# Optimization experiments

Measured on AMD Instinct MI355X. Metric: run time of the kernel, lower is better.

The kernel has to match this reference:

```python
import jax, jax.numpy as jnp
import numpy as np

B, L, D, NLAYERS, MAX_NODES, DEG = 32, 512, 768, 3, 128, 8


def _build_graph():
    rng = np.random.default_rng(0)
    per = rng.integers(-32, 33, size=B // 2)
    sizes = np.concatenate([96 + per, 96 - per]).astype(np.int64)  # sum = 96*B = 3072, each in [64,128]
    N = int(sizes.sum())
    offs = np.concatenate([[0], np.cumsum(sizes)])
    batch = np.repeat(np.arange(B), sizes).astype(np.int64)
    pad_idx = np.zeros((B, MAX_NODES), np.int64)
    pad_mask = np.zeros((B, MAX_NODES), bool)
    src, dst = [], []
    for b in range(B):
        n = int(sizes[b])
        pad_idx[b, :n] = np.arange(offs[b], offs[b] + n)
        pad_mask[b, :n] = True
        src.append(rng.integers(offs[b], offs[b] + n, n * DEG))
        dst.append(rng.integers(offs[b], offs[b] + n, n * DEG))
    return N, batch, pad_idx, pad_mask, np.concatenate(src), np.concatenate(dst)


def setup_inputs() -> dict:
    N, batch, pad_idx, pad_mask, esrc, edst = _build_graph()
    key = jax.random.key(0)
    ks = jax.random.split(key, 8)
    s = 1.0 / np.sqrt(D)
    return {
        "x": jax.random.normal(ks[0], (N, D), jnp.float32),
        "text": jax.random.normal(ks[1], (B, L, D), jnp.float32),
        "batch_ent1_d_mask": jnp.ones((B, 1), jnp.float32),
        "batch_ent1_g_mask": jnp.ones((B, 1), jnp.float32),
        "gnn_ws": jax.random.normal(ks[2], (NLAYERS, D, D), jnp.float32) * s,
        "gnn_wn": jax.random.normal(ks[3], (NLAYERS, D, D), jnp.float32) * s,
        "gnn_b": jnp.zeros((NLAYERS, D), jnp.float32),
        "atom_w": jax.random.normal(ks[4], (D, D), jnp.float32) * s,
        "atom_b": jnp.zeros((D,), jnp.float32),
        "rand_emb": jax.random.normal(ks[5], (1, D), jnp.float32),
        "batch": jnp.asarray(batch),
        "pad_idx": jnp.asarray(pad_idx),
        "pad_mask": jnp.asarray(pad_mask),
        "edge_src": jnp.asarray(esrc),
        "edge_dst": jnp.asarray(edst),
    }


def reference(x, text, batch_ent1_d_mask, batch_ent1_g_mask, gnn_ws, gnn_wn, gnn_b,
              atom_w, atom_b, rand_emb, batch, pad_idx, pad_mask, edge_src, edge_dst):
    N = x.shape[0]
    E = edge_src.shape[0]
    maskf = pad_mask.astype(x.dtype)            # [B, M]
    n_per = maskf.sum(axis=1)                   # [B] num real nodes per graph
    # edge-neighbor mean counts (constants w.r.t. x)
    cnt = jax.ops.segment_sum(jnp.ones((E,), x.dtype), edge_dst, num_segments=N)
    inv_cnt = 1.0 / jnp.maximum(cnt, 1.0)
    cms = []
    for i in range(NLAYERS):
        # MoleGraphConv stand-in: mean neighbor aggregation + self transform
        msg = jax.ops.segment_sum(x[edge_src], edge_dst, num_segments=N) * inv_cnt[:, None]
        x = jax.nn.relu(x @ gnn_ws[i] + msg @ gnn_wn[i] + gnn_b[i])
        # ragged gather into padded [B, M, D]
        xp = x[pad_idx] * maskf[..., None]
        # graph -> text cross attention (softmax over text tokens; no mask needed)
        g2t = jax.nn.softmax(jnp.einsum('bmd,bld->bml', xp, text), axis=-1)
        g2t_out = jnp.einsum('bml,bld->bmd', g2t, text)            # [B, M, D]
        # text -> graph cross attention (mask padded nodes)
        t2g_logits = jnp.einsum('bld,bmd->blm', text, xp)
        t2g_logits = jnp.where(pad_mask[:, None, :], t2g_logits, jnp.float32(-1e9))
        t2g = jax.nn.softmax(t2g_logits, axis=-1)
        t2g_out = jnp.einsum('blm,bmd->bld', t2g, xp)              # [B, L, D]
        # mean over concatenated rows [n_i + L] per graph (pool_type=2)
        pooled = ((g2t_out * maskf[..., None]).sum(axis=1) + t2g_out.sum(axis=1)) \
                 / (n_per + jnp.float32(L))[:, None]
        cms.append(pooled)
    out_cms = jnp.mean(jnp.stack(cms, axis=1), axis=1)              # mean over layers
    out_t = text[:, 0, :]
    # scatter-mean of final node features per graph
    gsum = jax.ops.segment_sum(x, batch, num_segments=B)
    gcnt = jax.ops.segment_sum(jnp.ones((N,), x.dtype), batch, num_segments=B)
    xg = gsum / jnp.maximum(gcnt, 1.0)[:, None]
    # dropout is a no-op in eval mode
    out_g = jnp.tanh(xg @ atom_w + atom_b)
    z = rand_emb[0]
    dg = batch_ent1_d_mask * batch_ent1_g_mask
    return jnp.concatenate([
        out_t * batch_ent1_d_mask + (1 - batch_ent1_d_mask) * z,
        out_g * batch_ent1_g_mask + (1 - batch_ent1_g_mask) * z,
        out_cms * dg + (1 - dg) * z,
    ], axis=-1)
```

## Files before the change

kernel.cpp:

```cpp
#include <hip/hip_runtime.h>

#define D 768
#define B 32
#define L 512
#define M 128
#define NNODES 3072
#define NEDGES 24576

using bf16x8 = __attribute__((ext_vector_type(8))) short;
using f32x4  = __attribute__((ext_vector_type(4))) float;

__device__ __forceinline__ float bf2f(unsigned short u) {
  union { unsigned int i; float f; } v; v.i = ((unsigned int)u) << 16; return v.f;
}
__device__ __forceinline__ unsigned short f2bf(float f) {
  union { float f; unsigned int i; } v; v.f = f;
  unsigned int x = v.i;
  return (unsigned short)((x + 0x7FFFu + ((x >> 16) & 1u)) >> 16);
}
__device__ __forceinline__ float ldf(const void* p, size_t i, int f32) {
  return f32 ? ((const float*)p)[i] : bf2f(((const unsigned short*)p)[i]);
}
__device__ __forceinline__ int ldi(const void* p, size_t i, int w64) {
  return w64 ? (int)((const long long*)p)[i] : ((const int*)p)[i];
}
__device__ __forceinline__ f32x4 mfma16(bf16x8 a, bf16x8 b, f32x4 c) {
  return __builtin_amdgcn_mfma_f32_16x16x32_bf16(a, b, c, 0, 0, 0);
}
__device__ __forceinline__ void gl_lds(const unsigned short* gsrc, unsigned short* lbase,
                                       int lane) {
  __builtin_amdgcn_global_load_lds(
      (const __attribute__((address_space(1))) unsigned int*)(gsrc + lane * 8),
      (__attribute__((address_space(3))) unsigned int*)lbase, 16, 0, 0);
}

__device__ __forceinline__ float pk_read(const unsigned short* P, int p, int l, int d) {
  return bf2f(P[(((size_t)(p * 24 + (d >> 5))) << 9) + ((((d & 31) >> 3) << 4) + l) * 8 + (d & 7)]);
}

__device__ __forceinline__ void fma8(float* acc, float w, uint4 v) {
  unsigned xs[4] = {v.x, v.y, v.z, v.w};
#pragma unroll
  for (int j = 0; j < 4; ++j) {
    acc[2 * j]     += w * bf2f((unsigned short)(xs[j] & 0xFFFFu));
    acc[2 * j + 1] += w * bf2f((unsigned short)(xs[j] >> 16));
  }
}


__device__ void d_pack_in(const void* src, unsigned short* rows, unsigned short* dst,
                          int p, int tid, int f) {
  unsigned short* pb = dst + (size_t)p * 12288;
#pragma unroll
  for (int j = 0; j < 6; ++j) {
    int odx = j * 256 + tid;
    int kk = odx >> 6, lanep = odx & 63;
    int q = lanep >> 4, r16 = lanep & 15;
    int row = p * 16 + r16, col0 = kk * 32 + q * 8;
    size_t sbase = (size_t)row * 768 + col0;
    union { unsigned short v[8]; uint4 qv; } u;
    if (f) {
      const float* sp = (const float*)src + sbase;
      float4 v0 = *(const float4*)sp;
      float4 v1 = *(const float4*)(sp + 4);
      u.v[0] = f2bf(v0.x); u.v[1] = f2bf(v0.y); u.v[2] = f2bf(v0.z); u.v[3] = f2bf(v0.w);
      u.v[4] = f2bf(v1.x); u.v[5] = f2bf(v1.y); u.v[6] = f2bf(v1.z); u.v[7] = f2bf(v1.w);
    } else {
      u.qv = *(const uint4*)((const unsigned short*)src + sbase);
    }
    if (rows) *(uint4*)&rows[sbase] = u.qv;
    *(uint4*)&pb[(size_t)odx * 8] = u.qv;
  }
}

__device__ void d_pack(const unsigned short* src, unsigned short* dst,
                       int p, int tid) {
  unsigned short* pb = dst + (size_t)p * 12288;
#pragma unroll
  for (int j = 0; j < 6; ++j) {
    int odx = j * 256 + tid;
    int kk = odx >> 6, lanep = odx & 63;
    int q = lanep >> 4, r16 = lanep & 15;
    size_t sbase = (size_t)(p * 16 + r16) * 768 + kk * 32 + q * 8;
    uint4 qv = *(const uint4*)(src + sbase);
    *(uint4*)&pb[(size_t)odx * 8] = qv;
  }
}

__device__ void d_wpack(const void* Ws, const void* Wn, const void* Aw, int f,
                        unsigned short* WsPk, unsigned short* WnPk, unsigned short* AwPk,
                        int r0, int tid, char* smem) {
  unsigned short* buf = (unsigned short*)smem;
  int z = r0 / 288, rem = r0 % 288;
  int nblk = rem % 12, kk = rem / 12;
  const void* src; unsigned short* dst; size_t zoff;
  if (z < 3)      { src = Ws; zoff = (size_t)z * D * D;       dst = WsPk + zoff; }
  else if (z < 6) { src = Wn; zoff = (size_t)(z - 3) * D * D; dst = WnPk + zoff; }
  else            { src = Aw; zoff = 0;                       dst = AwPk; }
  int n0 = nblk * 64;
  int kl = tid >> 3, c8 = tid & 7;
  size_t sbase = zoff + (size_t)(kk * 32 + kl) * D + n0 + c8 * 8;
  unsigned short v[8];
  if (f) {
    const float* sp = (const float*)src + sbase;
#pragma unroll
    for (int e = 0; e < 8; ++e) v[e] = f2bf(sp[e]);
  } else {
    const unsigned short* sp = (const unsigned short*)src + sbase;
#pragma unroll
    for (int e = 0; e < 8; ++e) v[e] = sp[e];
  }
  int ebit = kl & 7, quad = kl >> 3;
#pragma unroll
  for (int i = 0; i < 8; ++i) {
    int nl = c8 * 8 + i;
    int pl = nl >> 4;
    int lane = quad * 16 + (nl & 15);
    buf[pl * 512 + lane * 8 + ebit] = v[i];
  }
  __syncthreads();
  int pl = tid >> 6, pos = tid & 63;
  int pG = nblk * 4 + pl;
  uint4 q = *(const uint4*)&buf[pl * 512 + pos * 8];
  *(uint4*)&dst[(((size_t)(pG * 24 + kk)) << 9) + pos * 8] = q;
}

__device__ void d_count(const void* edst, const void* batch, int w,
                        int* cnt, int* gcnt, int i) {
  if (i < NEDGES) atomicAdd(&cnt[ldi(edst, i, w)], 1);
  if (i < NNODES) atomicAdd(&gcnt[ldi(batch, i, w)], 1);
}

__device__ void d_msg(const unsigned short* x, const int* cnt, const int* rowstart,
                      const int* csr, unsigned short* Mpk, int p, int tid) {
  int w = tid >> 6, lane = tid & 63;
  unsigned short* pb = Mpk + (size_t)p * 12288;
#pragma unroll
  for (int i = 0; i < 4; ++i) {
    int r = w * 4 + i;
    int n = p * 16 + r;
    int deg = cnt[n], base = rowstart[n];
    float inv = 1.0f / (float)(deg > 1 ? deg : 1);
    float a[12];
#pragma unroll
    for (int j = 0; j < 12; ++j) a[j] = 0.f;
    for (int e = 0; e < deg; ++e) {
      const uint2* xr = (const uint2*)(x + (size_t)csr[base + e] * D);
#pragma unroll
      for (int j = 0; j < 3; ++j) {
        uint2 v = xr[lane + j * 64];
        a[j * 4 + 0] += bf2f((unsigned short)(v.x & 0xFFFFu));
        a[j * 4 + 1] += bf2f((unsigned short)(v.x >> 16));
        a[j * 4 + 2] += bf2f((unsigned short)(v.y & 0xFFFFu));
        a[j * 4 + 3] += bf2f((unsigned short)(v.y >> 16));
      }
    }
#pragma unroll
    for (int j = 0; j < 3; ++j) {
      int d0 = (lane + j * 64) * 4;
      int kk = d0 >> 5, q = (d0 >> 3) & 3, e0 = d0 & 7;
      unsigned int lo = (unsigned int)f2bf(a[j * 4 + 0] * inv)
                      | ((unsigned int)f2bf(a[j * 4 + 1] * inv) << 16);
      unsigned int hi = (unsigned int)f2bf(a[j * 4 + 2] * inv)
                      | ((unsigned int)f2bf(a[j * 4 + 3] * inv) << 16);
      uint2 wv; wv.x = lo; wv.y = hi;
      *(uint2*)&pb[kk * 512 + (q * 16 + r) * 8 + e0] = wv;
    }
  }
}

__device__ void d_gemm(const unsigned short* Xpk, const unsigned short* Mpk,
                       const unsigned short* WsPk, const unsigned short* WnPk,
                       const void* bias, size_t bias_off, int f,
                       unsigned short* Y, int bx, int by, int tid, char* smem) {
  unsigned short* lds = (unsigned short*)smem;
  int wave = tid >> 6, lane = tid & 63;
  int q = lane >> 4, t = lane & 15;
  int wm = wave >> 1, wn = wave & 1;
  int pa = bx * 4, pb = by * 4;
  f32x4 acc[2][2];
#pragma unroll
  for (int mi = 0; mi < 2; ++mi)
#pragma unroll
    for (int ni = 0; ni < 2; ++ni)
      acc[mi][ni] = (f32x4){0.f, 0.f, 0.f, 0.f};
  int c0 = wave * 2;
  int pan0 = (wave < 2) ? (pa + c0) : (pb + c0 - 4);
  auto issue = [&](int r) {
    unsigned short* dbuf = &lds[(r % 3) * 8192 + c0 * 512];
#pragma unroll
    for (int st = 0; st < 2; ++st) {
      int s = r * 2 + st;
      int h = (s >= 24) ? 1 : 0;
      const unsigned short* P = (wave < 2) ? (h ? Mpk : Xpk) : (h ? WnPk : WsPk);
      int kk = s - h * 24;
      gl_lds(P + (((size_t)(pan0 * 24 + kk)) << 9), dbuf + st * 4096, lane);
      gl_lds(P + (((size_t)((pan0 + 1) * 24 + kk)) << 9), dbuf + st * 4096 + 512, lane);
    }
  };
  issue(0);
  issue(1);
  for (int r = 0; r < 24; ++r) {
    if (r < 23) asm volatile("s_waitcnt vmcnt(4)" ::: "memory");
    else        asm volatile("s_waitcnt vmcnt(0)" ::: "memory");
    __builtin_amdgcn_s_barrier();
    asm volatile("" ::: "memory");
    if (r < 22) issue(r + 2);
    const unsigned short* bb = &lds[(r % 3) * 8192];
#pragma unroll
    for (int st = 0; st < 2; ++st) {
      const unsigned short* bs = bb + st * 4096;
      bf16x8 a0 = *(const bf16x8*)&bs[(wm * 2 + 0) * 512 + lane * 8];
      bf16x8 a1 = *(const bf16x8*)&bs[(wm * 2 + 1) * 512 + lane * 8];
      bf16x8 b0 = *(const bf16x8*)&bs[(4 + wn * 2 + 0) * 512 + lane * 8];
      bf16x8 b1 = *(const bf16x8*)&bs[(4 + wn * 2 + 1) * 512 + lane * 8];
      acc[0][0] = mfma16(a0, b0, acc[0][0]);
      acc[0][1] = mfma16(a0, b1, acc[0][1]);
      acc[1][0] = mfma16(a1, b0, acc[1][0]);
      acc[1][1] = mfma16(a1, b1, acc[1][1]);
    }
    asm volatile("" ::: "memory");
  }
#pragma unroll
  for (int ni = 0; ni < 2; ++ni) {
    int col = by * 64 + wn * 32 + ni * 16 + t;
    float bv = ldf(bias, bias_off + col, f);
#pragma unroll
    for (int mi = 0; mi < 2; ++mi) {
#pragma unroll
      for (int r = 0; r < 4; ++r) {
        int row = bx * 64 + wm * 32 + mi * 16 + q * 4 + r;
        float v = acc[mi][ni][r] + bv;
        Y[(size_t)row * D + col] = f2bf(v > 0.f ? v : 0.f);
      }
    }
  }
}

__device__ void d_xp(const unsigned short* Xn, const void* pidx, int w64,
                     const int* gcnt, unsigned short* xp, unsigned short* XpPk,
                     float* xgacc, int p, int tid, char* smem) {
  unsigned short* rows = (unsigned short*)smem;
  int r = tid >> 4, c16 = tid & 15;
  int bm = p * 16 + r;
  int b = bm >> 7, m = bm & 127;
  int nb = gcnt[b];
  uint4* dl = (uint4*)&rows[r * 776];
  if (m < nb) {
    const uint4* srcr = (const uint4*)(Xn + (size_t)ldi(pidx, bm, w64) * D);
#pragma unroll
    for (int j = 0; j < 6; ++j) dl[c16 + j * 16] = srcr[c16 + j * 16];
  } else {
    uint4 z = {0u, 0u, 0u, 0u};
#pragma unroll
    for (int j = 0; j < 6; ++j) dl[c16 + j * 16] = z;
  }
  __syncthreads();
#pragma unroll
  for (int j = 0; j < 6; ++j) {
    int idx = j * 256 + tid;
    int rr = idx / 96, cc = idx % 96;
    uint4 vv = *(const uint4*)&rows[rr * 776 + cc * 8];
    *(uint4*)&xp[(size_t)(p * 16 + rr) * D + cc * 8] = vv;
  }
  unsigned short* pb = XpPk + (size_t)p * 12288;
#pragma unroll
  for (int j = 0; j < 6; ++j) {
    int odx = j * 256 + tid;
    int kk = odx >> 6, lanep = odx & 63;
    int rr = lanep & 15, cg = lanep >> 4;
    int cc = kk * 4 + cg;
    uint4 vv = *(const uint4*)&rows[rr * 776 + cc * 8];
    *(uint4*)&pb[odx * 8] = vv;
  }
  if (xgacc) {
    int bb = p >> 3;
#pragma unroll
    for (int j = 0; j < 3; ++j) {
      int d = j * 256 + tid;
      float s = 0.f;
#pragma unroll
      for (int rr = 0; rr < 16; ++rr) s += bf2f(rows[rr * 776 + d]);
      atomicAdd(&xgacc[(size_t)bb * D + d], s);
    }
  }
}

__device__ void d_scores(const unsigned short* XpPk, const unsigned short* Tpk,
                         float* S, int bx, int by, int bz, int tid, char* smem) {
  unsigned short* lds = (unsigned short*)smem;
  int wave = tid >> 6, lane = tid & 63;
  int q = lane >> 4, t = lane & 15;
  int wm = wave >> 1, wn = wave & 1;
  int pa = bz * 8 + bx * 4;
  int pb = bz * 32 + by * 4;
  f32x4 acc[2][2];
#pragma unroll
  for (int mi = 0; mi < 2; ++mi)
#pragma unroll
    for (int ni = 0; ni < 2; ++ni)
      acc[mi][ni] = (f32x4){0.f, 0.f, 0.f, 0.f};
  int c0 = wave * 2;
  const unsigned short* P = (wave < 2) ? XpPk : Tpk;
  int pan0 = (wave < 2) ? (pa + c0) : (pb + c0 - 4);
  auto issue = [&](int r) {
    unsigned short* dbuf = &lds[(r % 3) * 8192 + c0 * 512];
#pragma unroll
    for (int st = 0; st < 2; ++st) {
      int kk = r * 2 + st;
      gl_lds(P + (((size_t)(pan0 * 24 + kk)) << 9), dbuf + st * 4096, lane);
      gl_lds(P + (((size_t)((pan0 + 1) * 24 + kk)) << 9), dbuf + st * 4096 + 512, lane);
    }
  };
  issue(0);
  issue(1);
  for (int r = 0; r < 12; ++r) {
    if (r < 11) asm volatile("s_waitcnt vmcnt(4)" ::: "memory");
    else        asm volatile("s_waitcnt vmcnt(0)" ::: "memory");
    __builtin_amdgcn_s_barrier();
    asm volatile("" ::: "memory");
    if (r < 10) issue(r + 2);
    const unsigned short* bb = &lds[(r % 3) * 8192];
#pragma unroll
    for (int st = 0; st < 2; ++st) {
      const unsigned short* bs = bb + st * 4096;
      bf16x8 a0 = *(const bf16x8*)&bs[(wm * 2 + 0) * 512 + lane * 8];
      bf16x8 a1 = *(const bf16x8*)&bs[(wm * 2 + 1) * 512 + lane * 8];
      bf16x8 b0 = *(const bf16x8*)&bs[(4 + wn * 2 + 0) * 512 + lane * 8];
      bf16x8 b1 = *(const bf16x8*)&bs[(4 + wn * 2 + 1) * 512 + lane * 8];
      acc[0][0] = mfma16(a0, b0, acc[0][0]);
      acc[0][1] = mfma16(a0, b1, acc[0][1]);
      acc[1][0] = mfma16(a1, b0, acc[1][0]);
      acc[1][1] = mfma16(a1, b1, acc[1][1]);
    }
    asm volatile("" ::: "memory");
  }
  float* Sb = S + (size_t)bz * M * L;
#pragma unroll
  for (int ni = 0; ni < 2; ++ni) {
    int col = by * 64 + wn * 32 + ni * 16 + t;
#pragma unroll
    for (int mi = 0; mi < 2; ++mi) {
#pragma unroll
      for (int r = 0; r < 4; ++r) {
        int row = bx * 64 + wm * 32 + mi * 16 + q * 4 + r;
        Sb[(size_t)row * L + col] = acc[mi][ni][r];
      }
    }
  }
}

__device__ void d_stats(const float* S, const int* gcnt, float* rmax, float* rsum,
                        float* cmaxv, float* csumv, int bid, int tid, char* smem) {
  if (bid < B * M) {
    float* red = (float*)smem;
    int lane = tid & 63, wv = tid >> 6;
    const float* r = S + (size_t)bid * L;
    float s0 = r[tid], s1 = r[tid + 256];
    float m = fmaxf(s0, s1);
#pragma unroll
    for (int o = 32; o > 0; o >>= 1) m = fmaxf(m, __shfl_down(m, o));
    if (lane == 0) red[wv] = m;
    __syncthreads();
    float bm = fmaxf(fmaxf(red[0], red[1]), fmaxf(red[2], red[3]));
    __syncthreads();
    float e = __expf(s0 - bm) + __expf(s1 - bm);
#pragma unroll
    for (int o = 32; o > 0; o >>= 1) e += __shfl_down(e, o);
    if (lane == 0) red[wv] = e;
    __syncthreads();
    if (tid == 0) { rmax[bid] = bm; rsum[bid] = red[0] + red[1] + red[2] + red[3]; }
  } else {
    float (*pm)[64] = (float(*)[64])smem;
    float (*ps)[64] = (float(*)[64])(smem + 1024);
    int cid = bid - B * M;
    int b = cid >> 3, ly = cid & 7;
    int w = tid >> 6, lane = tid & 63;
    int l = ly * 64 + lane;
    int nb = gcnt[b];
    const float* Sb = S + (size_t)b * M * L;
    int m0 = w * 32, m1 = min(m0 + 32, nb);
    float cm = -1e30f, cs = 0.f;
    for (int m = m0; m < m1; ++m) {
      float s = Sb[(size_t)m * L + l];
      if (s > cm) { cs = cs * __expf(cm - s) + 1.f; cm = s; }
      else cs += __expf(s - cm);
    }
    pm[w][lane] = cm; ps[w][lane] = cs;
    __syncthreads();
    if (w == 0) {
      float CM = -1e30f;
#pragma unroll
      for (int j = 0; j < 4; ++j) CM = fmaxf(CM, pm[j][lane]);
      float CS = 0.f;
#pragma unroll
      for (int j = 0; j < 4; ++j) CS += ps[j][lane] * __expf(pm[j][lane] - CM);
      cmaxv[b * L + l] = CM; csumv[b * L + l] = CS;
    }
  }
}

__device__ void d_cross(const float* S, const float* rmax, const float* rsum,
                        const float* cmaxv, const float* csumv, const int* gcnt,
                        float* wv, float* t2gcol, int bid, int tid, char* smem) {
  if (bid < 256) {
    float* rm = (float*)smem;
    float* ri = (float*)(smem + 512);
    float (*pw)[64] = (float(*)[64])(smem + 1024);
    int b = bid >> 3, ly = bid & 7;
    int w = tid >> 6, lane = tid & 63;
    if (tid < M) { rm[tid] = rmax[b * M + tid]; ri[tid] = 1.f / rsum[b * M + tid]; }
    __syncthreads();
    int l = ly * 64 + lane;
    int nb = gcnt[b];
    const float* Sb = S + (size_t)b * M * L;
    int m0 = w * 32, m1 = min(m0 + 32, nb);
    float wp = 0.f;
    for (int m = m0; m < m1; ++m)
      wp += __expf(Sb[(size_t)m * L + l] - rm[m]) * ri[m];
    pw[w][lane] = wp;
    __syncthreads();
    if (w == 0)
      wv[b * L + l] = pw[0][lane] + pw[1][lane] + pw[2][lane] + pw[3][lane];
  } else {
    float* red = (float*)smem;
    int bm = bid - 256;
    int b = bm >> 7, m = bm & 127;
    int lane = tid & 63, w = tid >> 6;
    int nb = gcnt[b];
    float acc = 0.f;
    if (m < nb) {
      const float* r = S + (size_t)bm * L;
      const float* cm = cmaxv + b * L;
      const float* cs = csumv + b * L;
      acc = __expf(r[tid] - cm[tid]) / cs[tid]
          + __expf(r[tid + 256] - cm[tid + 256]) / cs[tid + 256];
    }
#pragma unroll
    for (int o = 32; o > 0; o >>= 1) acc += __shfl_down(acc, o);
    if (lane == 0) red[w] = acc;
    __syncthreads();
    if (tid == 0) t2gcol[bm] = red[0] + red[1] + red[2] + red[3];
  }
}

__device__ void d_pooled(const float* wv, const float* t2gcol, const unsigned short* Tpk,
                         const unsigned short* xp, const int* gcnt, float* pooled,
                         int bid, int tid, char* smem) {
  float* lred = (float*)smem;
  float* wbuf = (float*)(smem + 3072);
  int b = bid / 10, seg = bid - b * 10;
  int chunk = tid % 96, half = tid / 96;
  int d = chunk * 8;
  float acc[8];
#pragma unroll
  for (int j = 0; j < 8; ++j) acc[j] = 0.f;
  if (tid < 64) {
    wbuf[tid] = (seg < 8) ? wv[b * L + seg * 64 + tid]
                          : t2gcol[b * M + (seg - 8) * 64 + tid];
  }
  __syncthreads();
  if (half < 2) {
    if (seg < 8) {
      int pbase = b * 32 + seg * 4;
      size_t cbase = ((size_t)(d >> 5)) << 9;
      int coff = ((d & 31) >> 3) << 4;
      for (int i = 0; i < 32; ++i) {
        int l = half * 32 + i;
        const unsigned short* src =
            Tpk + (((size_t)((pbase + (l >> 4)) * 24)) << 9) + cbase +
            (size_t)(coff + (l & 15)) * 8;
        fma8(acc, wbuf[l], *(const uint4*)src);
      }
    } else {
      const unsigned short* Xb = xp + (size_t)b * M * D + d;
      int m0 = (seg - 8) * 64;
      for (int i = 0; i < 32; ++i) {
        int mm = half * 32 + i;
        fma8(acc, wbuf[mm], *(const uint4*)&Xb[(size_t)(m0 + mm) * D]);
      }
    }
  }
  if (half == 1) {
#pragma unroll
    for (int j = 0; j < 8; ++j) lred[chunk * 8 + j] = acc[j];
  }
  __syncthreads();
  if (half == 0) {
    float inv = 1.f / ((float)gcnt[b] + 512.f);
#pragma unroll
    for (int j = 0; j < 8; ++j)
      atomicAdd(&pooled[(size_t)b * D + d + j], (acc[j] + lred[chunk * 8 + j]) * inv);
  }
}

__device__ void d_atom(const float* xgacc, const int* gcnt, const unsigned short* AwPk,
                       float* gpre, int bid, int tid) {
  int w = tid >> 6, lane = tid & 63;
  int q = lane >> 4, t = lane & 15;
  int nbase = bid * 64 + w * 16;
  int pb = nbase >> 4;
  int n0 = gcnt[t], n1 = gcnt[16 + t];
  float inv0 = 1.f / (float)(n0 > 1 ? n0 : 1);
  float inv1 = 1.f / (float)(n1 > 1 ? n1 : 1);
  f32x4 acc[2];
  acc[0] = (f32x4){0.f, 0.f, 0.f, 0.f};
  acc[1] = (f32x4){0.f, 0.f, 0.f, 0.f};
  for (int kk = 0; kk < 24; ++kk) {
    const float* s0 = xgacc + (size_t)t * D + kk * 32 + q * 8;
    const float* s1 = xgacc + (size_t)(16 + t) * D + kk * 32 + q * 8;
    union { unsigned short v[8]; bf16x8 f; } a0, a1;
#pragma unroll
    for (int j = 0; j < 8; ++j) { a0.v[j] = f2bf(s0[j] * inv0); a1.v[j] = f2bf(s1[j] * inv1); }
    bf16x8 bv = *(const bf16x8*)(AwPk + (((size_t)(pb * 24 + kk)) << 9) + (lane << 3));
    acc[0] = mfma16(a0.f, bv, acc[0]);
    acc[1] = mfma16(a1.f, bv, acc[1]);
  }
#pragma unroll
  for (int mi = 0; mi < 2; ++mi)
#pragma unroll
    for (int r = 0; r < 4; ++r) {
      int row = mi * 16 + q * 4 + r;
      gpre[(size_t)row * D + nbase + t] = acc[mi][r];
    }
}


__global__ void k_init(int* cnt, int* cursor, int* gcnt, float* pooled, float* xgacc,
                       const unsigned short* __restrict__ t,
                       const unsigned int* __restrict__ e, int* __restrict__ flags) {
  int i = blockIdx.x * 256 + threadIdx.x;
  if (i < NNODES) { cnt[i] = 0; cursor[i] = 0; }
  if (i < B) gcnt[i] = 0;
  if (i < B * D) { pooled[i] = 0.f; xgacc[i] = 0.f; }
  if (blockIdx.x == 0) {
    __shared__ int r0[256];
    __shared__ unsigned r1[256];
    int tid = threadIdx.x;
    int bad = 0;
    for (int j = tid; j < 8192; j += 256) {
      unsigned short u = t[2 * j];
      unsigned ex = (u >> 7) & 0xFF;
      if (ex >= 0xC0) bad = 1;
    }
    unsigned o = 0;
    for (int j = tid; j < NEDGES / 2; j += 256) o |= e[2 * j + 1];
    r0[tid] = bad; r1[tid] = o;
    __syncthreads();
    for (int s = 128; s > 0; s >>= 1) {
      if (tid < s) { r0[tid] |= r0[tid + s]; r1[tid] |= r1[tid + s]; }
      __syncthreads();
    }
    if (tid == 0) { flags[0] = r0[0]; flags[1] = (r1[0] == 0) ? 1 : 0; }
  }
}

__global__ __launch_bounds__(256) void k_setup2(
    const void* x_in, unsigned short* x0, unsigned short* PkA,
    const void* text, unsigned short* Tpk,
    const void* Ws, const void* Wn, const void* Aw,
    unsigned short* WsPk, unsigned short* WnPk, unsigned short* AwPk,
    const void* edst, const void* batch, int* cnt, int* gcnt,
    const int* __restrict__ flags) {
  extern __shared__ char smem[];
  int bid = blockIdx.x, tid = threadIdx.x;
  if (bid < 1216) {
    int f = flags[0];
    if (bid < NNODES / 16) d_pack_in(x_in, x0, PkA, bid, tid, f);
    else d_pack_in(text, nullptr, Tpk, bid - NNODES / 16, tid, f);
  } else if (bid < 3232) {
    d_wpack(Ws, Wn, Aw, flags[0], WsPk, WnPk, AwPk, bid - 1216, tid, smem);
  } else {
    d_count(edst, batch, flags[1], cnt, gcnt, (bid - 3232) * 256 + tid);
  }
}

__global__ void k_scan(const int* __restrict__ cnt, int* __restrict__ rowstart) {
  __shared__ int a[NNODES], b[NNODES];
  int tid = threadIdx.x;
  for (int i = tid; i < NNODES; i += 1024) a[i] = cnt[i];
  __syncthreads();
  int* s = a; int* d = b;
  for (int off = 1; off < NNODES; off <<= 1) {
    for (int i = tid; i < NNODES; i += 1024)
      d[i] = s[i] + (i >= off ? s[i - off] : 0);
    __syncthreads();
    int* t = s; s = d; d = t;
  }
  for (int i = tid; i < NNODES; i += 1024) rowstart[i + 1] = s[i];
  if (tid == 0) rowstart[0] = 0;
}

__global__ void k_scatter(const void* __restrict__ esrc, const void* __restrict__ edst,
                          const int* __restrict__ flags, const int* __restrict__ rowstart,
                          int* __restrict__ cursor, int* __restrict__ csr) {
  int w = flags[1];
  int i = blockIdx.x * 256 + threadIdx.x;
  if (i < NEDGES) {
    int dd = ldi(edst, i, w);
    int pos = atomicAdd(&cursor[dd], 1);
    csr[rowstart[dd] + pos] = ldi(esrc, i, w);
  }
}

__global__ __launch_bounds__(256) void k_msgp(
    const unsigned short* x, const int* cnt, const int* rowstart, const int* csr,
    unsigned short* Mpk) {
  d_msg(x, cnt, rowstart, csr, Mpk, blockIdx.x, threadIdx.x);
}

__device__ __forceinline__ void gemm_map(int g, int& bx, int& by) {
  int gs = (g % 8) * 72 + g / 8;
  bx = gs / 12; by = gs % 12;
}
__device__ __forceinline__ void sc_map(int g, int& bx, int& by, int& bz) {
  int gs = (g % 8) * 64 + g / 8;
  bx = gs & 1; by = (gs >> 1) & 7; bz = gs >> 4;
}

__global__ __launch_bounds__(256) void k_gemm(
    const unsigned short* Apk, const unsigned short* Mpk,
    const unsigned short* WsPk, const unsigned short* WnPk,
    const void* bias, unsigned long bias_off, const int* flags, unsigned short* Y) {
  extern __shared__ char smem[];
  int bx, by; gemm_map(blockIdx.x, bx, by);
  d_gemm(Apk, Mpk, WsPk, WnPk, bias, bias_off, flags[0], Y, bx, by,
         threadIdx.x, smem);
}

__global__ __launch_bounds__(256) void k_postg(
    const unsigned short* Y, unsigned short* Npk, int packN,
    const void* pidx, const int* flags, const int* gcnt,
    unsigned short* xp, unsigned short* XpPk, float* xgacc) {
  extern __shared__ char smem[];
  int bid = blockIdx.x, tid = threadIdx.x;
  if (bid < packN) d_pack(Y, Npk, bid, tid);
  else d_xp(Y, pidx, flags[1], gcnt, xp, XpPk, xgacc, bid - packN, tid, smem);
}

__global__ __launch_bounds__(256) void k_scmsg(
    const unsigned short* XpPk, const unsigned short* Tpk, float* S,
    int msgN, const unsigned short* x, const int* cnt, const int* rowstart,
    const int* csr, unsigned short* Mpk) {
  extern __shared__ char smem[];
  int bid = blockIdx.x, tid = threadIdx.x;
  if (bid < 512) {
    int bx, by, bz; sc_map(bid, bx, by, bz);
    d_scores(XpPk, Tpk, S, bx, by, bz, tid, smem);
  } else d_msg(x, cnt, rowstart, csr, Mpk, bid - 512, tid);
}

__global__ __launch_bounds__(256) void k_stgemm(
    const float* S, const int* gcnt, float* rmax, float* rsum, float* cmaxv, float* csumv,
    int gemmN, const unsigned short* Apk, const unsigned short* Mpk,
    const unsigned short* WsPk, const unsigned short* WnPk,
    const void* bias, unsigned long bias_off, const int* flags, unsigned short* Y) {
  extern __shared__ char smem[];
  int bid = blockIdx.x, tid = threadIdx.x;
  if (bid < 4352) d_stats(S, gcnt, rmax, rsum, cmaxv, csumv, bid, tid, smem);
  else {
    int bx, by; gemm_map(bid - 4352, bx, by);
    d_gemm(Apk, Mpk, WsPk, WnPk, bias, bias_off, flags[0], Y, bx, by, tid, smem);
  }
}

__global__ __launch_bounds__(256) void k_crpostg(
    const float* S, const float* rmax, const float* rsum, const float* cmaxv,
    const float* csumv, const int* gcnt, float* wv, float* t2gcol,
    int packN, int xpN, const unsigned short* Y, unsigned short* Npk,
    const void* pidx, const int* flags, unsigned short* xp, unsigned short* XpPk,
    float* xgacc) {
  extern __shared__ char smem[];
  int bid = blockIdx.x, tid = threadIdx.x;
  if (bid < 4352) d_cross(S, rmax, rsum, cmaxv, csumv, gcnt, wv, t2gcol, bid, tid, smem);
  else {
    int r = bid - 4352;
    if (r < packN) d_pack(Y, Npk, r, tid);
    else d_xp(Y, pidx, flags[1], gcnt, xp, XpPk, xgacc, r - packN, tid, smem);
  }
}

__global__ __launch_bounds__(256) void k_plscmsg(
    const float* wv, const float* t2gcol, const unsigned short* Tpk,
    const unsigned short* xpL, const int* gcnt, float* pooled,
    int scN, const unsigned short* XpPk, float* S,
    int msgN, const unsigned short* x, const int* cnt, const int* rowstart,
    const int* csr, unsigned short* Mpk,
    int atomN, const float* xgacc, const unsigned short* AwPk, float* gpre) {
  extern __shared__ char smem[];
  int bid = blockIdx.x, tid = threadIdx.x;
  if (bid < 320) { d_pooled(wv, t2gcol, Tpk, xpL, gcnt, pooled, bid, tid, smem); return; }
  int r = bid - 320;
  if (r < scN) {
    int bx, by, bz; sc_map(r, bx, by, bz);
    d_scores(XpPk, Tpk, S, bx, by, bz, tid, smem); return;
  }
  r -= scN;
  if (r < msgN) { d_msg(x, cnt, rowstart, csr, Mpk, r, tid); return; }
  d_atom(xgacc, gcnt, AwPk, gpre, r - msgN, tid);
}

__global__ __launch_bounds__(256) void k_final(
    const unsigned short* __restrict__ Tpk, const float* __restrict__ gpre,
    const float* __restrict__ pooled, const void* __restrict__ ab,
    const void* __restrict__ dmask, const void* __restrict__ gmask,
    const void* __restrict__ remb, const int* __restrict__ flags,
    void* __restrict__ out) {
  int f = flags[0];
  int b = blockIdx.x, tid = threadIdx.x;
  float dm = ldf(dmask, b, f);
  float gm = ldf(gmask, b, f);
  float dg = dm * gm;
  size_t base = (size_t)b * 2304;
#pragma unroll
  for (int j = 0; j < 3; ++j) {
    int d = tid + j * 256;
    float z = ldf(remb, d, f);
    float tv = pk_read(Tpk, b * 32, 0, d);
    float o0 = tv * dm + (1.f - dm) * z;
    float gv = tanhf(gpre[(size_t)b * D + d] + ldf(ab, d, f));
    float o1 = gv * gm + (1.f - gm) * z;
    float p = pooled[(size_t)b * D + d] * (1.f / 3.f);
    float o2 = p * dg + (1.f - dg) * z;
    if (f) {
      float* of = (float*)out;
      of[base + d] = o0; of[base + 768 + d] = o1; of[base + 1536 + d] = o2;
    } else {
      unsigned short* ob = (unsigned short*)out;
      ob[base + d] = f2bf(o0); ob[base + 768 + d] = f2bf(o1); ob[base + 1536 + d] = f2bf(o2);
    }
  }
}

extern "C" void kernel_launch(void* const* d_in, const int* in_sizes, int n_in,
                              void* d_out, int out_size, void* d_ws, size_t ws_size,
                              hipStream_t stream) {
  const void* x_in  = d_in[0];
  const void* text  = d_in[1];
  const void* dmask = d_in[2];
  const void* gmask = d_in[3];
  const void* gws   = d_in[4];
  const void* gwn   = d_in[5];
  const void* gb    = d_in[6];
  const void* aw    = d_in[7];
  const void* ab    = d_in[8];
  const void* remb  = d_in[9];
  const void* batch = d_in[10];
  const void* pidx  = d_in[11];
  const void* esrc  = d_in[13];
  const void* edst  = d_in[14];

  char* wsp = (char*)d_ws;
  size_t off = 0;
  auto carve = [&](size_t bytes) -> void* {
    void* p = wsp + off;
    off += (bytes + 255) & ~(size_t)255;
    return p;
  };
  int* flags = (int*)carve(2 * 4);
  unsigned short* x0    = (unsigned short*)carve((size_t)NNODES * D * 2);
  unsigned short* xA    = (unsigned short*)carve((size_t)NNODES * D * 2);
  unsigned short* xB    = (unsigned short*)carve((size_t)NNODES * D * 2);
  unsigned short* PkA   = (unsigned short*)carve((size_t)NNODES * D * 2);
  unsigned short* PkB   = (unsigned short*)carve((size_t)NNODES * D * 2);
  unsigned short* Mpk   = (unsigned short*)carve((size_t)NNODES * D * 2);
  unsigned short* Tpk   = (unsigned short*)carve((size_t)B * L * D * 2);
  unsigned short* WsPk  = (unsigned short*)carve((size_t)3 * D * D * 2);
  unsigned short* WnPk  = (unsigned short*)carve((size_t)3 * D * D * 2);
  unsigned short* AwPk  = (unsigned short*)carve((size_t)D * D * 2);
  unsigned short* xpA   = (unsigned short*)carve((size_t)B * M * D * 2);
  unsigned short* xpB   = (unsigned short*)carve((size_t)B * M * D * 2);
  unsigned short* XpPkA = (unsigned short*)carve((size_t)B * M * D * 2);
  unsigned short* XpPkB = (unsigned short*)carve((size_t)B * M * D * 2);
  float* xgacc   = (float*)carve((size_t)B * D * 4);
  float* gpre    = (float*)carve((size_t)B * D * 4);
  float* S       = (float*)carve((size_t)B * M * L * 4);
  float* rmax    = (float*)carve((size_t)B * M * 4);
  float* rsum    = (float*)carve((size_t)B * M * 4);
  float* wv      = (float*)carve((size_t)B * L * 4);
  float* cmaxv   = (float*)carve((size_t)B * L * 4);
  float* csumv   = (float*)carve((size_t)B * L * 4);
  float* t2gcol  = (float*)carve((size_t)B * M * 4);
  float* pooled  = (float*)carve((size_t)B * D * 4);
  int* cnt      = (int*)carve((size_t)NNODES * 4);
  int* rowstart = (int*)carve((size_t)(NNODES + 1) * 4);
  int* cursor   = (int*)carve((size_t)NNODES * 4);
  int* gcnt     = (int*)carve((size_t)B * 4);
  int* csr      = (int*)carve((size_t)NEDGES * 4);

  const size_t DD = (size_t)D * D;

  k_init<<<96, 256, 0, stream>>>(cnt, cursor, gcnt, pooled, xgacc,
                                 (const unsigned short*)text, (const unsigned int*)edst, flags);
  k_setup2<<<3328, 256, 4096, stream>>>(x_in, x0, PkA, text, Tpk, gws, gwn, aw,
                                        WsPk, WnPk, AwPk, edst, batch, cnt, gcnt, flags);
  k_scan<<<1, 1024, 0, stream>>>(cnt, rowstart);
  k_scatter<<<96, 256, 0, stream>>>(esrc, edst, flags, rowstart, cursor, csr);

  k_msgp<<<192, 256, 0, stream>>>(x0, cnt, rowstart, csr, Mpk);
  k_gemm<<<576, 256, 49152, stream>>>(PkA, Mpk, WsPk, WnPk, gb, 0, flags, xA);
  k_postg<<<448, 256, 24832, stream>>>(xA, PkB, 192, pidx, flags, gcnt, xpA, XpPkA, nullptr);
  k_scmsg<<<704, 256, 49152, stream>>>(XpPkA, Tpk, S, 192, xA, cnt, rowstart, csr, Mpk);
  k_stgemm<<<4928, 256, 49152, stream>>>(S, gcnt, rmax, rsum, cmaxv, csumv,
                                         576, PkB, Mpk, WsPk + DD, WnPk + DD, gb, D, flags, xB);
  k_crpostg<<<4800, 256, 24832, stream>>>(S, rmax, rsum, cmaxv, csumv, gcnt, wv, t2gcol,
                                          192, 256, xB, PkA, pidx, flags, xpB, XpPkB, nullptr);
  k_plscmsg<<<1024, 256, 49152, stream>>>(wv, t2gcol, Tpk, xpA, gcnt, pooled,
                                          512, XpPkB, S, 192, xB, cnt, rowstart, csr, Mpk,
                                          0, nullptr, nullptr, nullptr);
  k_stgemm<<<4928, 256, 49152, stream>>>(S, gcnt, rmax, rsum, cmaxv, csumv,
                                         576, PkA, Mpk, WsPk + 2 * DD, WnPk + 2 * DD,
                                         gb, 2 * D, flags, xA);
  k_crpostg<<<4608, 256, 24832, stream>>>(S, rmax, rsum, cmaxv, csumv, gcnt, wv, t2gcol,
                                          0, 256, xA, nullptr, pidx, flags, xpA, XpPkA, xgacc);
  k_plscmsg<<<832, 256, 49152, stream>>>(wv, t2gcol, Tpk, xpB, gcnt, pooled,
                                         512, XpPkA, S, 0, nullptr, nullptr, nullptr,
                                         nullptr, nullptr, 0, nullptr, nullptr, nullptr);
  k_stgemm<<<4352, 256, 2048, stream>>>(S, gcnt, rmax, rsum, cmaxv, csumv,
                                        0, nullptr, nullptr, nullptr, nullptr,
                                        nullptr, 0, flags, nullptr);
  k_crpostg<<<4352, 256, 2048, stream>>>(S, rmax, rsum, cmaxv, csumv, gcnt, wv, t2gcol,
                                         0, 0, nullptr, nullptr, pidx, flags,
                                         nullptr, nullptr, nullptr);
  k_plscmsg<<<332, 256, 4096, stream>>>(wv, t2gcol, Tpk, xpA, gcnt, pooled,
                                        0, nullptr, nullptr, 0, nullptr, nullptr, nullptr,
                                        nullptr, nullptr, 12, xgacc, AwPk, gpre);
  k_final<<<32, 256, 0, stream>>>(Tpk, gpre, pooled, ab, dmask, gmask, remb, flags, d_out);
}
```

Baseline: 422.5 us.

## Batch loads for memory parallelism, drop LDS in weight pack, reorder fused block roles

Pack routines now issue all global loads into registers before converting and storing, which raises the number of loads in flight. The weight-pack transpose reads strided columns directly instead of staging through LDS with a barrier, so k_setup2 no longer needs dynamic shared memory. Message aggregation now processes two nodes at once with interleaved neighbor loads. The order of block roles inside the fused kernels changes so that long or latency-bound work (msg, gemm, pack/xp) is scheduled first. In exchange, register pressure rises, and the strided weight reads may coalesce poorly.

After: 434.0 us. 2.7% more time.

```diff
diff --git a/kernel.cpp b/kernel.cpp
--- a/kernel.cpp
+++ b/kernel.cpp
@@ -47,82 +47,99 @@
   }
 }
 
+__device__ __forceinline__ void acc12(float* a, const uint2* u) {
+#pragma unroll
+  for (int j = 0; j < 3; ++j) {
+    a[j * 4 + 0] += bf2f((unsigned short)(u[j].x & 0xFFFFu));
+    a[j * 4 + 1] += bf2f((unsigned short)(u[j].x >> 16));
+    a[j * 4 + 2] += bf2f((unsigned short)(u[j].y & 0xFFFFu));
+    a[j * 4 + 3] += bf2f((unsigned short)(u[j].y >> 16));
+  }
+}
+
 
 __device__ void d_pack_in(const void* src, unsigned short* rows, unsigned short* dst,
                           int p, int tid, int f) {
   unsigned short* pb = dst + (size_t)p * 12288;
+  uint4 qv[6];
+  if (f) {
+    float4 v0[6], v1[6];
+#pragma unroll
+    for (int j = 0; j < 6; ++j) {
+      int odx = j * 256 + tid;
+      int kk = odx >> 6, lanep = odx & 63;
+      size_t sbase = (size_t)(p * 16 + (lanep & 15)) * 768 + kk * 32 + ((lanep >> 4) << 3);
+      const float* sp = (const float*)src + sbase;
+      v0[j] = *(const float4*)sp;
+      v1[j] = *(const float4*)(sp + 4);
+    }
+#pragma unroll
+    for (int j = 0; j < 6; ++j) {
+      union { unsigned short v[8]; uint4 q; } u;
+      u.v[0] = f2bf(v0[j].x); u.v[1] = f2bf(v0[j].y); u.v[2] = f2bf(v0[j].z); u.v[3] = f2bf(v0[j].w);
+      u.v[4] = f2bf(v1[j].x); u.v[5] = f2bf(v1[j].y); u.v[6] = f2bf(v1[j].z); u.v[7] = f2bf(v1[j].w);
+      qv[j] = u.q;
+    }
+  } else {
+#pragma unroll
+    for (int j = 0; j < 6; ++j) {
+      int odx = j * 256 + tid;
+      int kk = odx >> 6, lanep = odx & 63;
+      size_t sbase = (size_t)(p * 16 + (lanep & 15)) * 768 + kk * 32 + ((lanep >> 4) << 3);
+      qv[j] = *(const uint4*)((const unsigned short*)src + sbase);
+    }
+  }
 #pragma unroll
   for (int j = 0; j < 6; ++j) {
     int odx = j * 256 + tid;
     int kk = odx >> 6, lanep = odx & 63;
-    int q = lanep >> 4, r16 = lanep & 15;
-    int row = p * 16 + r16, col0 = kk * 32 + q * 8;
-    size_t sbase = (size_t)row * 768 + col0;
-    union { unsigned short v[8]; uint4 qv; } u;
-    if (f) {
-      const float* sp = (const float*)src + sbase;
-      float4 v0 = *(const float4*)sp;
-      float4 v1 = *(const float4*)(sp + 4);
-      u.v[0] = f2bf(v0.x); u.v[1] = f2bf(v0.y); u.v[2] = f2bf(v0.z); u.v[3] = f2bf(v0.w);
-      u.v[4] = f2bf(v1.x); u.v[5] = f2bf(v1.y); u.v[6] = f2bf(v1.z); u.v[7] = f2bf(v1.w);
-    } else {
-      u.qv = *(const uint4*)((const unsigned short*)src + sbase);
-    }
-    if (rows) *(uint4*)&rows[sbase] = u.qv;
-    *(uint4*)&pb[(size_t)odx * 8] = u.qv;
+    size_t sbase = (size_t)(p * 16 + (lanep & 15)) * 768 + kk * 32 + ((lanep >> 4) << 3);
+    if (rows) *(uint4*)&rows[sbase] = qv[j];
+    *(uint4*)&pb[(size_t)odx * 8] = qv[j];
   }
 }
 
 __device__ void d_pack(const unsigned short* src, unsigned short* dst,
                        int p, int tid) {
   unsigned short* pb = dst + (size_t)p * 12288;
+  uint4 qv[6];
 #pragma unroll
   for (int j = 0; j < 6; ++j) {
     int odx = j * 256 + tid;
     int kk = odx >> 6, lanep = odx & 63;
-    int q = lanep >> 4, r16 = lanep & 15;
-    size_t sbase = (size_t)(p * 16 + r16) * 768 + kk * 32 + q * 8;
-    uint4 qv = *(const uint4*)(src + sbase);
-    *(uint4*)&pb[(size_t)odx * 8] = qv;
+    size_t sbase = (size_t)(p * 16 + (lanep & 15)) * 768 + kk * 32 + ((lanep >> 4) << 3);
+    qv[j] = *(const uint4*)(src + sbase);
+  }
+#pragma unroll
+  for (int j = 0; j < 6; ++j) {
+    *(uint4*)&pb[(size_t)(j * 256 + tid) * 8] = qv[j];
   }
 }
 
 __device__ void d_wpack(const void* Ws, const void* Wn, const void* Aw, int f,
                         unsigned short* WsPk, unsigned short* WnPk, unsigned short* AwPk,
-                        int r0, int tid, char* smem) {
-  unsigned short* buf = (unsigned short*)smem;
+                        int r0, int tid) {
   int z = r0 / 288, rem = r0 % 288;
   int nblk = rem % 12, kk = rem / 12;
   const void* src; unsigned short* dst; size_t zoff;
   if (z < 3)      { src = Ws; zoff = (size_t)z * D * D;       dst = WsPk + zoff; }
   else if (z < 6) { src = Wn; zoff = (size_t)(z - 3) * D * D; dst = WnPk + zoff; }
   else            { src = Aw; zoff = 0;                       dst = AwPk; }
-  int n0 = nblk * 64;
-  int kl = tid >> 3, c8 = tid & 7;
-  size_t sbase = zoff + (size_t)(kk * 32 + kl) * D + n0 + c8 * 8;
-  unsigned short v[8];
+  int pl = tid >> 6, lane = tid & 63;
+  int pG = nblk * 4 + pl;
+  int k0 = kk * 32 + ((lane >> 4) << 3);
+  int n  = nblk * 64 + pl * 16 + (lane & 15);
+  union { unsigned short v[8]; uint4 q; } u;
   if (f) {
-    const float* sp = (const float*)src + sbase;
-#pragma unroll
-    for (int e = 0; e < 8; ++e) v[e] = f2bf(sp[e]);
+    const float* sp = (const float*)src + zoff + (size_t)k0 * D + n;
+#pragma unroll
+    for (int e = 0; e < 8; ++e) u.v[e] = f2bf(sp[(size_t)e * D]);
   } else {
-    const unsigned short* sp = (const unsigned short*)src + sbase;
-#pragma unroll
-    for (int e = 0; e < 8; ++e) v[e] = sp[e];
-  }
-  int ebit = kl & 7, quad = kl >> 3;
-#pragma unroll
-  for (int i = 0; i < 8; ++i) {
-    int nl = c8 * 8 + i;
-    int pl = nl >> 4;
-    int lane = quad * 16 + (nl & 15);
-    buf[pl * 512 + lane * 8 + ebit] = v[i];
-  }
-  __syncthreads();
-  int pl = tid >> 6, pos = tid & 63;
-  int pG = nblk * 4 + pl;
-  uint4 q = *(const uint4*)&buf[pl * 512 + pos * 8];
-  *(uint4*)&dst[(((size_t)(pG * 24 + kk)) << 9) + pos * 8] = q;
+    const unsigned short* sp = (const unsigned short*)src + zoff + (size_t)k0 * D + n;
+#pragma unroll
+    for (int e = 0; e < 8; ++e) u.v[e] = sp[(size_t)e * D];
+  }
+  *(uint4*)&dst[(((size_t)(pG * 24 + kk)) << 9) + lane * 8] = u.q;
 }
 
 __device__ void d_count(const void* edst, const void* batch, int w,
@@ -136,35 +153,45 @@
   int w = tid >> 6, lane = tid & 63;
   unsigned short* pb = Mpk + (size_t)p * 12288;
 #pragma unroll
-  for (int i = 0; i < 4; ++i) {
-    int r = w * 4 + i;
-    int n = p * 16 + r;
-    int deg = cnt[n], base = rowstart[n];
-    float inv = 1.0f / (float)(deg > 1 ? deg : 1);
-    float a[12];
-#pragma unroll
-    for (int j = 0; j < 12; ++j) a[j] = 0.f;
-    for (int e = 0; e < deg; ++e) {
-      const uint2* xr = (const uint2*)(x + (size_t)csr[base + e] * D);
-#pragma unroll
-      for (int j = 0; j < 3; ++j) {
-        uint2 v = xr[lane + j * 64];
-        a[j * 4 + 0] += bf2f((unsigned short)(v.x & 0xFFFFu));
-        a[j * 4 + 1] += bf2f((unsigned short)(v.x >> 16));
-        a[j * 4 + 2] += bf2f((unsigned short)(v.y & 0xFFFFu));
-        a[j * 4 + 3] += bf2f((unsigned short)(v.y >> 16));
+  for (int i = 0; i < 4; i += 2) {
+    int rA = w * 4 + i, rB = rA + 1;
+    int nA = p * 16 + rA, nB = p * 16 + rB;
+    int degA = cnt[nA], baseA = rowstart[nA];
+    int degB = cnt[nB], baseB = rowstart[nB];
+    float aA[12], aB[12];
+#pragma unroll
+    for (int j = 0; j < 12; ++j) { aA[j] = 0.f; aB[j] = 0.f; }
+    int dmax = degA > degB ? degA : degB;
+    for (int e = 0; e < dmax; ++e) {
+      uint2 uA[3], uB[3];
+      if (e < degA) {
+        const uint2* xr = (const uint2*)(x + (size_t)csr[baseA + e] * D);
+        uA[0] = xr[lane]; uA[1] = xr[lane + 64]; uA[2] = xr[lane + 128];
       }
-    }
+      if (e < degB) {
+        const uint2* xr = (const uint2*)(x + (size_t)csr[baseB + e] * D);
+        uB[0] = xr[lane]; uB[1] = xr[lane + 64]; uB[2] = xr[lane + 128];
+      }
+      if (e < degA) acc12(aA, uA);
+      if (e < degB) acc12(aB, uB);
+    }
+    float invA = 1.0f / (float)(degA > 1 ? degA : 1);
+    float invB = 1.0f / (float)(degB > 1 ? degB : 1);
 #pragma unroll
     for (int j = 0; j < 3; ++j) {
       int d0 = (lane + j * 64) * 4;
       int kk = d0 >> 5, q = (d0 >> 3) & 3, e0 = d0 & 7;
-      unsigned int lo = (unsigned int)f2bf(a[j * 4 + 0] * inv)
-                      | ((unsigned int)f2bf(a[j * 4 + 1] * inv) << 16);
-      unsigned int hi = (unsigned int)f2bf(a[j * 4 + 2] * inv)
-                      | ((unsigned int)f2bf(a[j * 4 + 3] * inv) << 16);
-      uint2 wv; wv.x = lo; wv.y = hi;
-      *(uint2*)&pb[kk * 512 + (q * 16 + r) * 8 + e0] = wv;
+      uint2 wA, wB;
+      wA.x = (unsigned int)f2bf(aA[j * 4 + 0] * invA)
+           | ((unsigned int)f2bf(aA[j * 4 + 1] * invA) << 16);
+      wA.y = (unsigned int)f2bf(aA[j * 4 + 2] * invA)
+           | ((unsigned int)f2bf(aA[j * 4 + 3] * invA) << 16);
+      wB.x = (unsigned int)f2bf(aB[j * 4 + 0] * invB)
+           | ((unsigned int)f2bf(aB[j * 4 + 1] * invB) << 16);
+      wB.y = (unsigned int)f2bf(aB[j * 4 + 2] * invB)
+           | ((unsigned int)f2bf(aB[j * 4 + 3] * invB) << 16);
+      *(uint2*)&pb[kk * 512 + (q * 16 + rA) * 8 + e0] = wA;
+      *(uint2*)&pb[kk * 512 + (q * 16 + rB) * 8 + e0] = wB;
     }
   }
 }
@@ -246,15 +273,18 @@
   int b = bm >> 7, m = bm & 127;
   int nb = gcnt[b];
   uint4* dl = (uint4*)&rows[r * 776];
+  uint4 v[6];
   if (m < nb) {
     const uint4* srcr = (const uint4*)(Xn + (size_t)ldi(pidx, bm, w64) * D);
 #pragma unroll
-    for (int j = 0; j < 6; ++j) dl[c16 + j * 16] = srcr[c16 + j * 16];
+    for (int j = 0; j < 6; ++j) v[j] = srcr[c16 + j * 16];
   } else {
     uint4 z = {0u, 0u, 0u, 0u};
 #pragma unroll
-    for (int j = 0; j < 6; ++j) dl[c16 + j * 16] = z;
-  }
+    for (int j = 0; j < 6; ++j) v[j] = z;
+  }
+#pragma unroll
+  for (int j = 0; j < 6; ++j) dl[c16 + j * 16] = v[j];
   __syncthreads();
 #pragma unroll
   for (int j = 0; j < 6; ++j) {
@@ -562,14 +592,13 @@
     unsigned short* WsPk, unsigned short* WnPk, unsigned short* AwPk,
     const void* edst, const void* batch, int* cnt, int* gcnt,
     const int* __restrict__ flags) {
-  extern __shared__ char smem[];
   int bid = blockIdx.x, tid = threadIdx.x;
   if (bid < 1216) {
     int f = flags[0];
     if (bid < NNODES / 16) d_pack_in(x_in, x0, PkA, bid, tid, f);
     else d_pack_in(text, nullptr, Tpk, bid - NNODES / 16, tid, f);
   } else if (bid < 3232) {
-    d_wpack(Ws, Wn, Aw, flags[0], WsPk, WnPk, AwPk, bid - 1216, tid, smem);
+    d_wpack(Ws, Wn, Aw, flags[0], WsPk, WnPk, AwPk, bid - 1216, tid);
   } else {
     d_count(edst, batch, flags[1], cnt, gcnt, (bid - 3232) * 256 + tid);
   }
@@ -634,8 +663,8 @@
     unsigned short* xp, unsigned short* XpPk, float* xgacc) {
   extern __shared__ char smem[];
   int bid = blockIdx.x, tid = threadIdx.x;
-  if (bid < packN) d_pack(Y, Npk, bid, tid);
-  else d_xp(Y, pidx, flags[1], gcnt, xp, XpPk, xgacc, bid - packN, tid, smem);
+  if (bid < 256) d_xp(Y, pidx, flags[1], gcnt, xp, XpPk, xgacc, bid, tid, smem);
+  else d_pack(Y, Npk, bid - 256, tid);
 }
 
 __global__ __launch_bounds__(256) void k_scmsg(
@@ -644,10 +673,11 @@
     const int* csr, unsigned short* Mpk) {
   extern __shared__ char smem[];
   int bid = blockIdx.x, tid = threadIdx.x;
-  if (bid < 512) {
-    int bx, by, bz; sc_map(bid, bx, by, bz);
+  if (bid < msgN) d_msg(x, cnt, rowstart, csr, Mpk, bid, tid);
+  else {
+    int bx, by, bz; sc_map(bid - msgN, bx, by, bz);
     d_scores(XpPk, Tpk, S, bx, by, bz, tid, smem);
-  } else d_msg(x, cnt, rowstart, csr, Mpk, bid - 512, tid);
+  }
 }
 
 __global__ __launch_bounds__(256) void k_stgemm(
@@ -657,11 +687,10 @@
     const void* bias, unsigned long bias_off, const int* flags, unsigned short* Y) {
   extern __shared__ char smem[];
   int bid = blockIdx.x, tid = threadIdx.x;
-  if (bid < 4352) d_stats(S, gcnt, rmax, rsum, cmaxv, csumv, bid, tid, smem);
-  else {
-    int bx, by; gemm_map(bid - 4352, bx, by);
+  if (bid < gemmN) {
+    int bx, by; gemm_map(bid, bx, by);
     d_gemm(Apk, Mpk, WsPk, WnPk, bias, bias_off, flags[0], Y, bx, by, tid, smem);
-  }
+  } else d_stats(S, gcnt, rmax, rsum, cmaxv, csumv, bid - gemmN, tid, smem);
 }
 
 __global__ __launch_bounds__(256) void k_crpostg(
@@ -672,12 +701,10 @@
     float* xgacc) {
   extern __shared__ char smem[];
   int bid = blockIdx.x, tid = threadIdx.x;
-  if (bid < 4352) d_cross(S, rmax, rsum, cmaxv, csumv, gcnt, wv, t2gcol, bid, tid, smem);
-  else {
-    int r = bid - 4352;
-    if (r < packN) d_pack(Y, Npk, r, tid);
-    else d_xp(Y, pidx, flags[1], gcnt, xp, XpPk, xgacc, r - packN, tid, smem);
-  }
+  if (bid < packN) { d_pack(Y, Npk, bid, tid); return; }
+  int r = bid - packN;
+  if (r < xpN) { d_xp(Y, pidx, flags[1], gcnt, xp, XpPk, xgacc, r, tid, smem); return; }
+  d_cross(S, rmax, rsum, cmaxv, csumv, gcnt, wv, t2gcol, r - xpN, tid, smem);
 }
 
 __global__ __launch_bounds__(256) void k_plscmsg(
@@ -689,15 +716,15 @@
     int atomN, const float* xgacc, const unsigned short* AwPk, float* gpre) {
   extern __shared__ char smem[];
   int bid = blockIdx.x, tid = threadIdx.x;
-  if (bid < 320) { d_pooled(wv, t2gcol, Tpk, xpL, gcnt, pooled, bid, tid, smem); return; }
-  int r = bid - 320;
+  if (bid < msgN) { d_msg(x, cnt, rowstart, csr, Mpk, bid, tid); return; }
+  int r = bid - msgN;
   if (r < scN) {
     int bx, by, bz; sc_map(r, bx, by, bz);
     d_scores(XpPk, Tpk, S, bx, by, bz, tid, smem); return;
   }
   r -= scN;
-  if (r < msgN) { d_msg(x, cnt, rowstart, csr, Mpk, r, tid); return; }
-  d_atom(xgacc, gcnt, AwPk, gpre, r - msgN, tid);
+  if (r < 320) { d_pooled(wv, t2gcol, Tpk, xpL, gcnt, pooled, r, tid, smem); return; }
+  d_atom(xgacc, gcnt, AwPk, gpre, r - 320, tid);
 }
 
 __global__ __launch_bounds__(256) void k_final(
@@ -792,8 +819,8 @@
 
   k_init<<<96, 256, 0, stream>>>(cnt, cursor, gcnt, pooled, xgacc,
                                  (const unsigned short*)text, (const unsigned int*)edst, flags);
-  k_setup2<<<3328, 256, 4096, stream>>>(x_in, x0, PkA, text, Tpk, gws, gwn, aw,
-                                        WsPk, WnPk, AwPk, edst, batch, cnt, gcnt, flags);
+  k_setup2<<<3328, 256, 0, stream>>>(x_in, x0, PkA, text, Tpk, gws, gwn, aw,
+                                     WsPk, WnPk, AwPk, edst, batch, cnt, gcnt, flags);
   k_scan<<<1, 1024, 0, stream>>>(cnt, rowstart);
   k_scatter<<<96, 256, 0, stream>>>(esrc, edst, flags, rowstart, cursor, csr);
 
```
